# Kernel tuning notes

Measured on AMD Instinct MI355X. Metric: run time of the kernel, lower is better.

Reference implementation:

```python
import jax, jax.numpy as jnp
import numpy as np
from jax import lax

B, T, H, C = 64, 512, 1024, 8


def setup_inputs() -> dict:
    key = jax.random.key(0)
    ks = jax.random.split(key, 7)
    encoding = jax.random.normal(ks[0], (B, T, H), dtype=jnp.float32)
    labels = jax.random.randint(ks[1], (B, 3 * T), 0, C)
    W = jax.random.normal(ks[2], (3, C, H), dtype=jnp.float32) * 0.02
    b = jax.random.normal(ks[3], (3, C), dtype=jnp.float32) * 0.02
    start_trans = jax.random.normal(ks[4], (3, C), dtype=jnp.float32) * 0.1
    end_trans = jax.random.normal(ks[5], (3, C), dtype=jnp.float32) * 0.1
    trans = jax.random.normal(ks[6], (3, C, C), dtype=jnp.float32) * 0.1
    return {"encoding": encoding, "labels": labels, "W": W, "b": b,
            "start_trans": start_trans, "end_trans": end_trans, "trans": trans}


def crf_neg_log_lik(em, tags, start, end, trans):
    # em [B,T,C], tags [B,T] -> scalar (torchcrf reduction='sum', loss = -llh)
    bsz = em.shape[0]
    # numerator: score of gold path
    em_sc = jnp.take_along_axis(em, tags[:, :, None], axis=2)[..., 0].sum(axis=1)
    tr_sc = trans[tags[:, :-1], tags[:, 1:]].sum(axis=1)
    num = start[tags[:, 0]] + em_sc + tr_sc + end[tags[:, -1]]
    # denominator: forward algorithm (log partition)
    a0 = start[None, :] + em[:, 0]  # [B,C]

    def step(a, e_t):
        a_new = jax.nn.logsumexp(a[:, :, None] + trans[None] + e_t[:, None, :], axis=1)
        return a_new, None

    aT, _ = lax.scan(step, a0, jnp.moveaxis(em[:, 1:], 1, 0))
    logZ = jax.nn.logsumexp(aT + end[None, :], axis=1)
    return -(num - logZ).sum()


def viterbi(em, start, end, trans):
    # em [B,T,C] -> best tag path [B,T] (no mask: all sequences full length)
    v0 = start[None, :] + em[:, 0]

    def step(v, e_t):
        s = v[:, :, None] + trans[None]          # [B,C_prev,C_cur]
        bp = jnp.argmax(s, axis=1)               # [B,C]
        return jnp.max(s, axis=1) + e_t, bp

    vT, bps = lax.scan(step, v0, jnp.moveaxis(em[:, 1:], 1, 0))  # bps [T-1,B,C]
    last = jnp.argmax(vT + end[None, :], axis=1)  # [B]

    def back(tag, bp):
        prev = jnp.take_along_axis(bp, tag[:, None], axis=1)[:, 0]
        return prev, prev

    _, rev = lax.scan(back, last, bps, reverse=True)  # [T-1,B], tags for t=0..T-2
    tags = jnp.concatenate([rev, last[None]], axis=0)  # [T,B]
    return tags.T


def reference(encoding, labels, W, b, start_trans, end_trans, trans):
    # three per-task projections: logits [3,B,T,C]
    logits = jnp.einsum('bth,kch->kbtc', encoding, W) + b[:, None, None, :]
    tags = jnp.stack(jnp.split(labels, 3, axis=1))  # [3,B,T] (task/process/material)
    losses = jax.vmap(crf_neg_log_lik)(logits, tags, start_trans, end_trans, trans)
    loss = losses.sum()
    pred = jax.vmap(viterbi)(logits, start_trans, end_trans, trans)  # [3,B,T]
    return loss, logits, pred
```

## Files before the change

### kernel.cpp

```cpp
#include <hip/hip_runtime.h>

#define NB 64
#define NT 512
#define NH 1024
#define NC 8
#define NK 3
#define BT (NB*NT)
#define LOGITS_N (NK*BT*NC)

#define QP1  0xB1
#define QP2  0x4E
#define ROR4 0x124
#define ROR8 0x128
#define HM   0x141

template<int CTRL>
__device__ __forceinline__ float dppf(float x) {
  return __int_as_float(__builtin_amdgcn_update_dpp(0, __float_as_int(x), CTRL, 0xF, 0xF, true));
}
template<int CTRL>
__device__ __forceinline__ int dppi(int x) {
  return __builtin_amdgcn_update_dpp(0, x, CTRL, 0xF, 0xF, true);
}

__global__ __launch_bounds__(256) void init_kernel(const float* __restrict__ W,
                                                   float* __restrict__ Wt,
                                                   float* __restrict__ out) {
  int i = blockIdx.x * 256 + threadIdx.x;
  if (i < 24 * NH) {
    int h = i / 24, j = i - h * 24;
    int kk = j >> 3, cc = j & 7;
    Wt[i] = W[kk * NC * NH + cc * NH + h];
  }
  if (i == 0) out[0] = 0.0f;
}

__global__ __launch_bounds__(256, 2) void proj_kernel(const float* __restrict__ enc,
                                                      const float* __restrict__ Wt,
                                                      const float* __restrict__ bias,
                                                      float* __restrict__ out) {
  __shared__ float smem[64 * 256];
  const int tid = threadIdx.x;
  const int lane = tid & 63;
  const int w = tid >> 6;
  const int row0 = blockIdx.x * 64;
  const int chrot = blockIdx.x & 3;
  const float* eb = enc + (size_t)row0 * 1024;

  float acc[24];
#pragma unroll
  for (int j = 0; j < 24; ++j) acc[j] = 0.0f;

  float4 pf[16];
  auto loadStage = [&](int ci) {
    const int cx = ci ^ chrot;
    const float* p = eb + (size_t)w * 1024 + cx * 256 + lane * 4;
#pragma unroll
    for (int i = 0; i < 16; ++i)
      pf[i] = *(const float4*)(p + (size_t)i * 4096);
  };
  auto writeStage = [&]() {
#pragma unroll
    for (int i = 0; i < 16; ++i) {
      const int r = i * 4 + w;
      const int slot = lane ^ (r & 7);
      *(float4*)&smem[r * 256 + slot * 4] = pf[i];
    }
  };

  loadStage(0);
  writeStage();

#pragma unroll 1
  for (int ch = 0; ch < 4; ++ch) {
    __syncthreads();
    if (ch < 3) loadStage(ch + 1);
    const int cx = ch ^ chrot;
    const float* wbase = Wt + __builtin_amdgcn_readfirstlane((cx * 256 + w * 64) * 24);
#pragma unroll 4
    for (int hh = 0; hh < 16; ++hh) {
      const int slot = (w * 16 + hh) ^ (lane & 7);
      float4 e4 = *(const float4*)&smem[lane * 256 + slot * 4];
      const float ev[4] = {e4.x, e4.y, e4.z, e4.w};
      const float* wr = wbase + hh * 96;
#pragma unroll
      for (int m = 0; m < 4; ++m) {
        const float e = ev[m];
        const float* wm = wr + m * 24;
#pragma unroll
        for (int j = 0; j < 24; ++j) acc[j] = fmaf(e, wm[j], acc[j]);
      }
    }
    __syncthreads();
    if (ch < 3) writeStage();
  }

  float* sp = smem + w * 1792;
#pragma unroll
  for (int j4 = 0; j4 < 24; j4 += 4)
    *(float4*)&sp[lane * 28 + j4] = make_float4(acc[j4], acc[j4+1], acc[j4+2], acc[j4+3]);
  __syncthreads();
  const int r = tid >> 2, j0 = (tid & 3) * 6;
#pragma unroll
  for (int u = 0; u < 6; ++u) {
    const int j = j0 + u;
    float s = smem[0 * 1792 + r * 28 + j] + smem[1 * 1792 + r * 28 + j]
            + smem[2 * 1792 + r * 28 + j] + smem[3 * 1792 + r * 28 + j] + bias[j];
    out[1 + (size_t)(j >> 3) * (BT * 8) + (size_t)(row0 + r) * 8 + (j & 7)] = s;
  }
}

__global__ __launch_bounds__(512) void crf_kernel(const int* __restrict__ labels,
                                                  const float* __restrict__ startT,
                                                  const float* __restrict__ endT,
                                                  const float* __restrict__ trans,
                                                  float* __restrict__ d_out) {
  __shared__ float sA[32 * 64];
  __shared__ float sVB[32 * 8];
  __shared__ int   sBP[512];
  __shared__ int   sMap[32 * 8];
  __shared__ int   sEnt[32];
  __shared__ float sRed[32];
  __shared__ unsigned char sTags[512];
  __shared__ int sTerm;

  const int tid = threadIdx.x;
  const int lane = tid & 63;
  const int w = tid >> 6;
  const int c = lane & 7;
  const int p = (lane >> 3) & 7;
  const int role = (blockIdx.x >= 192);
  const int seq = role ? blockIdx.x - 192 : blockIdx.x;
  const int k = seq >> 6, b = seq & 63;
  const float* em = d_out + 1 + ((size_t)k * BT + (size_t)b * 512) * 8;
  const float* trk = trans + k * 64;
  const int* lab = labels + b * (NK * NT) + k * NT;

  float Txc[8];
#pragma unroll
  for (int kk = 0; kk < 8; ++kk) Txc[kk] = trk[(c ^ kk) * 8 + c];
  const float Tpc = trk[p * 8 + c];
  const float startc = startT[k * 8 + c];
  const float endc = endT[k * 8 + c];

  if (!role) {
    float Mxc[8];
#pragma unroll
    for (int kk = 0; kk < 8; ++kk) Mxc[kk] = __expf(Txc[kk]);

#pragma unroll 1
    for (int it = 0; it < 4; ++it) {
      const int i = w * 4 + it;
      const int t0 = i * 16;
      const int te = (t0 + 16 < 512) ? (t0 + 16) : 511;
      float EX[16];
      EX[0] = em[(t0 + 1) * 8 + c];
#pragma unroll
      for (int j = 1; j < 16; ++j) {
        int t = t0 + 1 + j;
        EX[j] = (t <= te) ? __expf(em[t * 8 + c]) : 1.0f;
      }
      float V = __expf(Tpc + EX[0]);
#pragma unroll
      for (int j = 1; j < 16; ++j) {
        int t = t0 + 1 + j;
        if (t <= te) {
          float x1 = dppf<QP1>(V), x2 = dppf<QP2>(V), x3 = dppf<QP2>(x1);
          float x7 = dppf<HM>(V), x6 = dppf<QP1>(x7), x5 = dppf<QP2>(x7), x4 = dppf<QP2>(x6);
          float s01 = fmaf(x1, Mxc[1], V * Mxc[0]);
          float s23 = fmaf(x3, Mxc[3], x2 * Mxc[2]);
          float s45 = fmaf(x5, Mxc[5], x4 * Mxc[4]);
          float s67 = fmaf(x7, Mxc[7], x6 * Mxc[6]);
          V = ((s01 + s23) + (s45 + s67)) * EX[j];
        }
        if (j == 8) V *= 0x1p-32f;
      }
      sA[i * 64 + lane] = V;
    }
    __syncthreads();

    float logZ = 0.0f;
    if (w == 0) {
      float al = __expf(startc + em[c]);
      float lz = 0.0f;
#pragma unroll 1
      for (int i = 0; i < 32; ++i) {
        const float* Ai = &sA[i * 64];
        float A0 = Ai[(c ^ 0) * 8 + c], A1 = Ai[(c ^ 1) * 8 + c];
        float A2 = Ai[(c ^ 2) * 8 + c], A3 = Ai[(c ^ 3) * 8 + c];
        float A4 = Ai[(c ^ 4) * 8 + c], A5 = Ai[(c ^ 5) * 8 + c];
        float A6 = Ai[(c ^ 6) * 8 + c], A7 = Ai[(c ^ 7) * 8 + c];
        float a1 = dppf<QP1>(al), a2 = dppf<QP2>(al), a3 = dppf<QP2>(a1);
        float a4 = dppf<ROR4>(al), a5 = dppf<ROR4>(a1), a6 = dppf<ROR4>(a2), a7 = dppf<ROR4>(a3);
        float s01 = fmaf(a1, A1, al * A0);
        float s23 = fmaf(a3, A3, a2 * A2);
        float s45 = fmaf(a5, A5, a4 * A4);
        float s67 = fmaf(a7, A7, a6 * A6);
        float s = (s01 + s23) + (s45 + s67);
        float ss = s;
        ss += dppf<QP1>(ss); ss += dppf<QP2>(ss); ss += dppf<ROR4>(ss);
        lz += __logf(ss);
        al = s * (1.0f / ss);
      }
      float se = al * __expf(endc);
      se += dppf<QP1>(se); se += dppf<QP2>(se); se += dppf<ROR4>(se);
      logZ = lz + __logf(se) + 1024.0f * 0.69314718055994531f;
    } else {
      int idx = (w - 1) * 64 + lane;
      float ns = 0.0f;
      {
        int tg = lab[idx];
        ns += em[(size_t)idx * 8 + tg] + trk[tg * 8 + lab[idx + 1]];
      }
      if (idx < 64) {
        int t = idx + 448;
        int tg = lab[t];
        ns += em[(size_t)t * 8 + tg];
        if (t < 511) ns += trk[tg * 8 + lab[t + 1]];
      }
      ns += dppf<QP1>(ns); ns += dppf<QP2>(ns); ns += dppf<HM>(ns); ns += dppf<ROR8>(ns);
      if ((lane & 15) == 0) sRed[(w - 1) * 4 + (lane >> 4)] = ns;
    }
    __syncthreads();
    if (tid == 0) {
      float num = startT[k * 8 + lab[0]] + endT[k * 8 + lab[511]];
#pragma unroll
      for (int u = 0; u < 28; ++u) num += sRed[u];
      atomicAdd(d_out, logZ - num);
    }
  } else {
#pragma unroll 1
    for (int it = 0; it < 4; ++it) {
      const int i = w * 4 + it;
      const int t0 = i * 16;
      const int te = (t0 + 16 < 512) ? (t0 + 16) : 511;
      float emv[16];
#pragma unroll
      for (int j = 0; j < 16; ++j) {
        int t = t0 + 1 + j;
        emv[j] = (t <= te) ? em[t * 8 + c] : 0.0f;
      }
      float V = Tpc + emv[0];
#pragma unroll
      for (int j = 1; j < 16; ++j) {
        int t = t0 + 1 + j;
        if (t <= te) {
          float x1 = dppf<QP1>(V), x2 = dppf<QP2>(V), x3 = dppf<QP2>(x1);
          float x7 = dppf<HM>(V), x6 = dppf<QP1>(x7), x5 = dppf<QP2>(x7), x4 = dppf<QP2>(x6);
          float c0 = V + Txc[0], c1 = x1 + Txc[1], c2 = x2 + Txc[2], c3 = x3 + Txc[3];
          float c4 = x4 + Txc[4], c5 = x5 + Txc[5], c6 = x6 + Txc[6], c7 = x7 + Txc[7];
          float m0 = fmaxf(fmaxf(c0, c1), c2);
          float m1 = fmaxf(fmaxf(c3, c4), c5);
          float m2 = fmaxf(c6, c7);
          V = fmaxf(fmaxf(m0, m1), m2) + emv[j];
        }
      }
      sA[i * 64 + lane] = V;
    }
    __syncthreads();

    if (w == 0) {
      float v = startc + em[c];
#pragma unroll 1
      for (int i = 0; i < 32; ++i) {
        if (lane < 8) sVB[i * 8 + c] = v;
        const float* Ai = &sA[i * 64];
        float A0 = Ai[(c ^ 0) * 8 + c], A1 = Ai[(c ^ 1) * 8 + c];
        float A2 = Ai[(c ^ 2) * 8 + c], A3 = Ai[(c ^ 3) * 8 + c];
        float A4 = Ai[(c ^ 4) * 8 + c], A5 = Ai[(c ^ 5) * 8 + c];
        float A6 = Ai[(c ^ 6) * 8 + c], A7 = Ai[(c ^ 7) * 8 + c];
        float a1 = dppf<QP1>(v), a2 = dppf<QP2>(v), a3 = dppf<QP2>(a1);
        float a4 = dppf<ROR4>(v), a5 = dppf<ROR4>(a1), a6 = dppf<ROR4>(a2), a7 = dppf<ROR4>(a3);
        float c0 = v + A0, c1 = a1 + A1, c2 = a2 + A2, c3 = a3 + A3;
        float c4 = a4 + A4, c5 = a5 + A5, c6 = a6 + A6, c7 = a7 + A7;
        float m0 = fmaxf(fmaxf(c0, c1), c2);
        float m1 = fmaxf(fmaxf(c3, c4), c5);
        float m2 = fmaxf(c6, c7);
        v = fmaxf(fmaxf(m0, m1), m2);
      }
      float lv = v + endc;
      int li = c;
      {
        float ov; int oi; bool take;
        ov = dppf<QP1>(lv); oi = dppi<QP1>(li);
        take = (ov > lv) || (ov == lv && oi < li); lv = take ? ov : lv; li = take ? oi : li;
        ov = dppf<QP2>(lv); oi = dppi<QP2>(li);
        take = (ov > lv) || (ov == lv && oi < li); lv = take ? ov : lv; li = take ? oi : li;
        ov = dppf<ROR4>(lv); oi = dppi<ROR4>(li);
        take = (ov > lv) || (ov == lv && oi < li); lv = take ? ov : lv; li = take ? oi : li;
      }
      if (lane == 0) sTerm = li;
    }
    __syncthreads();

    if (w < 4) {
      const int u = lane >> 3;
      const int i = w * 8 + u;
      const int t0 = i * 16;
      const int te = (t0 + 16 < 512) ? (t0 + 16) : 511;
      float emv[16];
#pragma unroll
      for (int j = 0; j < 16; ++j) {
        int t = t0 + 1 + j;
        emv[j] = (t <= te) ? em[t * 8 + c] : 0.0f;
      }
      float v = sVB[i * 8 + c];
#pragma unroll
      for (int j = 0; j < 16; ++j) {
        int t = t0 + 1 + j;
        if (t <= te) {
          float x1 = dppf<QP1>(v), x2 = dppf<QP2>(v), x3 = dppf<QP2>(x1);
          float x7 = dppf<HM>(v), x6 = dppf<QP1>(x7), x5 = dppf<QP2>(x7), x4 = dppf<QP2>(x6);
          float c0 = v + Txc[0], c1 = x1 + Txc[1], c2 = x2 + Txc[2], c3 = x3 + Txc[3];
          float c4 = x4 + Txc[4], c5 = x5 + Txc[5], c6 = x6 + Txc[6], c7 = x7 + Txc[7];
          float m0 = fmaxf(fmaxf(c0, c1), c2);
          float m1 = fmaxf(fmaxf(c3, c4), c5);
          float m2 = fmaxf(c6, c7);
          float best = fmaxf(fmaxf(m0, m1), m2);
          int a0 = (c0 == best) ? (c ^ 0) : 8;
          int a1i = (c1 == best) ? (c ^ 1) : 8;
          int a2i = (c2 == best) ? (c ^ 2) : 8;
          int a3i = (c3 == best) ? (c ^ 3) : 8;
          int a4i = (c4 == best) ? (c ^ 4) : 8;
          int a5i = (c5 == best) ? (c ^ 5) : 8;
          int a6i = (c6 == best) ? (c ^ 6) : 8;
          int a7i = (c7 == best) ? (c ^ 7) : 8;
          int arg = min(min(min(a0, a1i), min(a2i, a3i)),
                        min(min(a4i, a5i), min(a6i, a7i)));
          v = best + emv[j];
          int wd = arg << (3 * c);
          wd |= dppi<QP1>(wd); wd |= dppi<QP2>(wd); wd |= dppi<HM>(wd);
          if ((lane & 7) == 0) sBP[t] = wd;
        }
      }
    }
    __syncthreads();

    if (w < 4) {
      const int u = lane >> 3;
      const int i = w * 8 + u;
      const int t0 = i * 16;
      const int te = (t0 + 16 < 512) ? (t0 + 16) : 511;
      int tag = c;
#pragma unroll
      for (int j = 16; j >= 1; --j) {
        int t = t0 + j;
        if (t <= te) tag = (sBP[t] >> (3 * tag)) & 7;
      }
      sMap[i * 8 + c] = tag;
    }
    __syncthreads();
    if (tid == 0) {
      int cur = sTerm;
#pragma unroll 1
      for (int i = 31; i >= 0; --i) { cur = sMap[i * 8 + cur]; sEnt[i] = cur; }
    }
    __syncthreads();
    if (w == 0 && lane < 32) {
      const int i = lane;
      const int t0 = i * 16;
      const int te = (t0 + 16 < 512) ? (t0 + 16) : 511;
      int tag = (i == 31) ? sTerm : sEnt[i + 1];
      if (i == 31) sTags[511] = (unsigned char)tag;
#pragma unroll
      for (int j = 16; j >= 1; --j) {
        int t = t0 + j;
        if (t <= te) { tag = (sBP[t] >> (3 * tag)) & 7; sTags[t - 1] = (unsigned char)tag; }
      }
    }
    __syncthreads();
    float* outp = d_out + 1 + LOGITS_N + (size_t)seq * 512;
    outp[tid] = (float)sTags[tid];
  }
}

extern "C" void kernel_launch(void* const* d_in, const int* in_sizes, int n_in,
                              void* d_out, int out_size, void* d_ws, size_t ws_size,
                              hipStream_t stream) {
  const float* enc    = (const float*)d_in[0];
  const int*   labels = (const int*)  d_in[1];
  const float* W      = (const float*)d_in[2];
  const float* bias   = (const float*)d_in[3];
  const float* startT = (const float*)d_in[4];
  const float* endT   = (const float*)d_in[5];
  const float* trans  = (const float*)d_in[6];
  float* out = (float*)d_out;
  float* Wt  = (float*)d_ws;

  init_kernel<<<dim3(96), dim3(256), 0, stream>>>(W, Wt, out);
  proj_kernel<<<dim3(512), dim3(256), 0, stream>>>(enc, Wt, bias, out);
  crf_kernel<<<dim3(384), dim3(512), 0, stream>>>(labels, startT, endT, trans, out);
}
```

Measured before the change: 272.8 us.

## Double-buffer projection tiles with direct global-to-LDS async loads

```diff
diff --git a/kernel.cpp b/kernel.cpp
--- a/kernel.cpp
+++ b/kernel.cpp
@@ -21,6 +21,12 @@
 template<int CTRL>
 __device__ __forceinline__ int dppi(int x) {
   return __builtin_amdgcn_update_dpp(0, x, CTRL, 0xF, 0xF, true);
+}
+
+__device__ __forceinline__ void gload_lds16(const float* g, float* l) {
+  __builtin_amdgcn_global_load_lds(
+      (const __attribute__((address_space(1))) void*)g,
+      (__attribute__((address_space(3))) void*)l, 16, 0, 0);
 }
 
 __global__ __launch_bounds__(256) void init_kernel(const float* __restrict__ W,
@@ -39,50 +45,40 @@
                                                       const float* __restrict__ Wt,
                                                       const float* __restrict__ bias,
                                                       float* __restrict__ out) {
-  __shared__ float smem[64 * 256];
+  __shared__ float smem[2 * 64 * 128];
   const int tid = threadIdx.x;
   const int lane = tid & 63;
   const int w = tid >> 6;
   const int row0 = blockIdx.x * 64;
-  const int chrot = blockIdx.x & 3;
+  const int chrot = blockIdx.x & 7;
   const float* eb = enc + (size_t)row0 * 1024;
 
   float acc[24];
 #pragma unroll
   for (int j = 0; j < 24; ++j) acc[j] = 0.0f;
 
-  float4 pf[16];
-  auto loadStage = [&](int ci) {
+  auto stage = [&](int ci, int buf) {
     const int cx = ci ^ chrot;
-    const float* p = eb + (size_t)w * 1024 + cx * 256 + lane * 4;
-#pragma unroll
-    for (int i = 0; i < 16; ++i)
-      pf[i] = *(const float4*)(p + (size_t)i * 4096);
+#pragma unroll
+    for (int i = 0; i < 8; ++i) {
+      const int r = w * 16 + 2 * i + (lane >> 5);
+      const int s = (lane & 31) ^ (r & 7);
+      const float* g = eb + (size_t)r * 1024 + cx * 128 + s * 4;
+      gload_lds16(g, &smem[buf * 8192 + (w * 16 + 2 * i) * 128]);
+    }
   };
-  auto writeStage = [&]() {
-#pragma unroll
-    for (int i = 0; i < 16; ++i) {
-      const int r = i * 4 + w;
-      const int slot = lane ^ (r & 7);
-      *(float4*)&smem[r * 256 + slot * 4] = pf[i];
-    }
-  };
-
-  loadStage(0);
-  writeStage();
-
-#pragma unroll 1
-  for (int ch = 0; ch < 4; ++ch) {
-    __syncthreads();
-    if (ch < 3) loadStage(ch + 1);
-    const int cx = ch ^ chrot;
-    const float* wbase = Wt + __builtin_amdgcn_readfirstlane((cx * 256 + w * 64) * 24);
-#pragma unroll 4
-    for (int hh = 0; hh < 16; ++hh) {
-      const int slot = (w * 16 + hh) ^ (lane & 7);
-      float4 e4 = *(const float4*)&smem[lane * 256 + slot * 4];
+
+  auto compute = [&](int ci, int buf) {
+    const int cx = ci ^ chrot;
+    const float* wbase = Wt + __builtin_amdgcn_readfirstlane((cx * 128 + w * 32) * 24);
+    const float* er = &smem[buf * 8192 + lane * 128];
+    const int rx = lane & 7;
+#pragma unroll
+    for (int hq = 0; hq < 8; ++hq) {
+      const int slot = (w * 8 + hq) ^ rx;
+      const float4 e4 = *(const float4*)&er[slot * 4];
       const float ev[4] = {e4.x, e4.y, e4.z, e4.w};
-      const float* wr = wbase + hh * 96;
+      const float* wr = wbase + hq * 96;
 #pragma unroll
       for (int m = 0; m < 4; ++m) {
         const float e = ev[m];
@@ -91,8 +87,24 @@
         for (int j = 0; j < 24; ++j) acc[j] = fmaf(e, wm[j], acc[j]);
       }
     }
-    __syncthreads();
-    if (ch < 3) writeStage();
+  };
+
+  stage(0, 0);
+
+#pragma unroll 1
+  for (int ci = 0; ci < 8; ++ci) {
+    const int buf = ci & 1;
+    if (ci < 7) {
+      stage(ci + 1, buf ^ 1);
+      asm volatile("s_waitcnt vmcnt(8)" ::: "memory");
+    } else {
+      asm volatile("s_waitcnt vmcnt(0)" ::: "memory");
+    }
+    __builtin_amdgcn_s_barrier();
+    asm volatile("" ::: "memory");
+    compute(ci, buf);
+    asm volatile("" ::: "memory");
+    __builtin_amdgcn_s_barrier();
   }
 
   float* sp = smem + w * 1792;
```

Result: no change. 268.3 us (-1.7%).
